# Optimization experiments

Measured on AMD Instinct MI355X. Metric: run time of the kernel, lower is better.

## Reference

```python
import jax, jax.numpy as jnp
import numpy as np

N_NODES = 50000
N_EDGES = 1000000
N_HID = 64
N_GRAPHS = 500
IN_DIM = 4


def setup_inputs() -> dict:
    key = jax.random.key(0)
    ks = jax.random.split(key, 10)
    x = jax.random.normal(ks[0], (N_NODES, IN_DIM), dtype=jnp.float32)
    edge_index = jax.random.randint(ks[1], (2, N_EDGES), 0, N_NODES, dtype=jnp.int64)
    batch = jnp.sort(jax.random.randint(ks[2], (N_NODES,), 0, N_GRAPHS, dtype=jnp.int64))
    # learned parameters (glorot-ish init)
    W1 = jax.random.normal(ks[3], (IN_DIM, N_HID), dtype=jnp.float32) / np.sqrt(IN_DIM)
    b1 = jnp.zeros((N_HID,), dtype=jnp.float32)
    W2 = jax.random.normal(ks[4], (N_HID, N_HID), dtype=jnp.float32) / np.sqrt(N_HID)
    b2 = jnp.zeros((N_HID,), dtype=jnp.float32)
    W3 = jax.random.normal(ks[5], (N_HID, 1), dtype=jnp.float32) / np.sqrt(N_HID)
    b3 = jnp.zeros((1,), dtype=jnp.float32)
    return {"x": x, "edge_index": edge_index, "batch": batch,
            "W1": W1, "b1": b1, "W2": W2, "b2": b2, "W3": W3, "b3": b3}


def gcn_conv(x, W, b, src, dst, num_nodes):
    """PyG GCNConv: x@W, add self-loops, sym deg^-1/2 norm, scatter-add aggregate, +bias."""
    h = x @ W  # [N, D]
    loop = jnp.arange(num_nodes, dtype=src.dtype)
    s = jnp.concatenate([src, loop])  # source nodes (messages gathered from)
    d = jnp.concatenate([dst, loop])  # target nodes (messages scattered to)
    deg = jax.ops.segment_sum(jnp.ones_like(d, dtype=h.dtype), d, num_segments=num_nodes)
    dis = jnp.where(deg > 0, jax.lax.rsqrt(jnp.maximum(deg, 1e-12)), 0.0)
    norm = dis[s] * dis[d]  # [E+N]
    msg = h[s] * norm[:, None]  # gather + scale: the memory-bound hot loop
    out = jax.ops.segment_sum(msg, d, num_segments=num_nodes)
    return out + b


def reference(x, edge_index, batch, W1, b1, W2, b2, W3, b3):
    src, dst = edge_index[0], edge_index[1]
    n = x.shape[0]
    h = gcn_conv(x, W1, b1, src, dst, n)
    h = jax.nn.elu(h)
    # F.dropout with training=False (eval mode) is identity
    h = gcn_conv(h, W2, b2, src, dst, n)
    h = jax.nn.elu(h)
    # scatter-mean pooling over graphs
    sums = jax.ops.segment_sum(h, batch, num_segments=N_GRAPHS)
    cnts = jax.ops.segment_sum(jnp.ones((n,), dtype=h.dtype), batch, num_segments=N_GRAPHS)
    pooled = sums / jnp.maximum(cnts, 1.0)[:, None]
    return pooled @ W3 + b3  # [N_GRAPHS, 1]
```

## Files before the change

### kernel.cpp

```cpp
#include <hip/hip_runtime.h>
#include <math.h>

#define N_NODES 50000
#define N_EDGES 1000000
#define N_HID 64
#define N_GRAPHS 500
#define IN_DIM 4
#define NPAD 50048

#define BK_SHIFT 7
#define BK_NODES 128
#define NBUCK 391
#define BCAP 3072
#define EPT 16
#define EPW (EPT * 256)
#define NWG_BIN ((N_EDGES + EPW - 1) / EPW)

__global__ void k_init(int* bcur, int* gstart, int* gend) {
    int i = threadIdx.x;
    if (i < 512) { bcur[i] = 0; gstart[i] = 0; gend[i] = 0; }
}

__global__ void k_bin(const int* __restrict__ ei, int* bcur, int* __restrict__ P) {
    __shared__ int hist[NBUCK];
    __shared__ int base[NBUCK];
    int t = threadIdx.x;
    int wg0 = blockIdx.x * EPW;
    for (int b = t; b < NBUCK; b += 256) hist[b] = 0;
    __syncthreads();

    const int4* s4 = (const int4*)ei;
    const int4* d4 = (const int4*)(ei + N_EDGES);
    int rs[EPT], rd[EPT];
#pragma unroll
    for (int i = 0; i < 4; ++i) {
        int e = wg0 + (i * 256 + t) * 4;
        if (e < N_EDGES) {
            int4 vs = s4[e >> 2];
            int4 vd = d4[e >> 2];
            rs[i * 4 + 0] = vs.x; rd[i * 4 + 0] = vd.x;
            rs[i * 4 + 1] = vs.y; rd[i * 4 + 1] = vd.y;
            rs[i * 4 + 2] = vs.z; rd[i * 4 + 2] = vd.z;
            rs[i * 4 + 3] = vs.w; rd[i * 4 + 3] = vd.w;
            atomicAdd(&hist[vd.x >> BK_SHIFT], 1);
            atomicAdd(&hist[vd.y >> BK_SHIFT], 1);
            atomicAdd(&hist[vd.z >> BK_SHIFT], 1);
            atomicAdd(&hist[vd.w >> BK_SHIFT], 1);
        } else {
            rd[i * 4 + 0] = rd[i * 4 + 1] = rd[i * 4 + 2] = rd[i * 4 + 3] = -1;
        }
    }
    __syncthreads();
    for (int b = t; b < NBUCK; b += 256) {
        int h = hist[b];
        base[b] = h ? atomicAdd(&bcur[b], h) : 0;
    }
    __syncthreads();
    for (int b = t; b < NBUCK; b += 256) hist[b] = 0;
    __syncthreads();
#pragma unroll
    for (int i = 0; i < EPT; ++i) {
        if (rd[i] >= 0) {
            int bk = rd[i] >> BK_SHIFT;
            int loc = base[bk] + atomicAdd(&hist[bk], 1);
            if (loc > BCAP - 1) loc = BCAP - 1;
            P[(size_t)bk * BCAP + loc] = (rs[i] << BK_SHIFT) | (rd[i] & (BK_NODES - 1));
        }
    }
}

__global__ void k_build(const int* __restrict__ bcur, const int* __restrict__ P,
                        const float* __restrict__ x,
                        int* __restrict__ srcidx, int* __restrict__ offs,
                        int* __restrict__ endp, float* __restrict__ dis,
                        float* __restrict__ xs) {
    __shared__ int sp[BCAP];
    __shared__ int scnt[BK_NODES];
    __shared__ int sscan[BK_NODES];
    __shared__ int scur[BK_NODES];
    int b = blockIdx.x;
    int t = threadIdx.x;
    int n = bcur[b];
    if (n > BCAP) n = BCAP;
    if (t < BK_NODES) scnt[t] = 0;
    __syncthreads();
    for (int i = t; i < n; i += 256) {
        int v = P[(size_t)b * BCAP + i];
        sp[i] = v;
        atomicAdd(&scnt[v & (BK_NODES - 1)], 1);
    }
    __syncthreads();
    if (t < BK_NODES) sscan[t] = scnt[t];
    __syncthreads();
    for (int d = 1; d < BK_NODES; d <<= 1) {
        int v = 0;
        if (t < BK_NODES && t >= d) v = sscan[t - d];
        __syncthreads();
        if (t < BK_NODES) sscan[t] += v;
        __syncthreads();
    }
    if (t < BK_NODES) {
        int excl = sscan[t] - scnt[t];
        scur[t] = excl;
        int node = b * BK_NODES + t;
        if (node < N_NODES) {
            int o = b * BCAP + excl;
            offs[node] = o;
            endp[node] = o + scnt[t];
            float dd = 1.0f / sqrtf((float)(scnt[t] + 1));
            dis[node] = dd;
            float4 xv = ((const float4*)x)[node];
            xv.x *= dd; xv.y *= dd; xv.z *= dd; xv.w *= dd;
            ((float4*)xs)[node] = xv;
        }
    }
    __syncthreads();
    for (int i = t; i < n; i += 256) {
        int v = sp[i];
        int ln = v & (BK_NODES - 1);
        int pos = b * BCAP + atomicAdd(&scur[ln], 1);
        srcidx[pos] = v >> BK_SHIFT;
    }
}

__global__ void k_layer1(const float* __restrict__ xs, const int* __restrict__ offs,
                         const int* __restrict__ endp, const int* __restrict__ srcidx,
                         const float* __restrict__ dis, const int* __restrict__ batch,
                         const float* __restrict__ W1, const float* __restrict__ b1,
                         int* __restrict__ gstart, int* __restrict__ gend,
                         float* __restrict__ h1s) {
    __shared__ float4 sagg[256];
    __shared__ float sdis[256];
    __shared__ float sW1[IN_DIM * N_HID];
    __shared__ float sb1[N_HID];
    int t = threadIdx.x;
    int nb = blockIdx.x * 256;
    int i = nb + t;
    sW1[t] = W1[t];
    if (t < N_HID) sb1[t] = b1[t];
    if (i < N_NODES) {
        int g = batch[i];
        if (i == 0 || batch[i - 1] != g) gstart[g] = i;
        if (i == N_NODES - 1 || batch[i + 1] != g) gend[g] = i + 1;
        const float4* xs4 = (const float4*)xs;
        float4 a0 = xs4[i];
        float4 a1 = make_float4(0.f, 0.f, 0.f, 0.f);
        float4 a2 = a1, a3 = a1;
        int q = offs[i], e = endp[i];
        for (; q + 4 <= e; q += 4) {
            int i0 = srcidx[q], i1 = srcidx[q + 1], i2 = srcidx[q + 2], i3 = srcidx[q + 3];
            float4 v0 = xs4[i0], v1 = xs4[i1], v2 = xs4[i2], v3 = xs4[i3];
            a0.x += v0.x; a0.y += v0.y; a0.z += v0.z; a0.w += v0.w;
            a1.x += v1.x; a1.y += v1.y; a1.z += v1.z; a1.w += v1.w;
            a2.x += v2.x; a2.y += v2.y; a2.z += v2.z; a2.w += v2.w;
            a3.x += v3.x; a3.y += v3.y; a3.z += v3.z; a3.w += v3.w;
        }
        for (; q < e; ++q) {
            float4 v = xs4[srcidx[q]];
            a0.x += v.x; a0.y += v.y; a0.z += v.z; a0.w += v.w;
        }
        float dd = dis[i];
        float4 r;
        r.x = (a0.x + a1.x + a2.x + a3.x) * dd;
        r.y = (a0.y + a1.y + a2.y + a3.y) * dd;
        r.z = (a0.z + a1.z + a2.z + a3.z) * dd;
        r.w = (a0.w + a1.w + a2.w + a3.w) * dd;
        sagg[t] = r;
        sdis[t] = dd;
    } else {
        sagg[t] = make_float4(0.f, 0.f, 0.f, 0.f);
        sdis[t] = 0.f;
    }
    __syncthreads();
    int w = t >> 6, j = t & 63;
    float w0 = sW1[0 * N_HID + j], w1 = sW1[1 * N_HID + j];
    float w2 = sW1[2 * N_HID + j], w3 = sW1[3 * N_HID + j];
    float bj = sb1[j];
    for (int n = 0; n < 64; ++n) {
        int local = w * 64 + n;
        int node = nb + local;
        if (node >= N_NODES) break;
        float4 a = sagg[local];
        float acc = a.x * w0 + a.y * w1 + a.z * w2 + a.w * w3 + bj;
        acc = acc > 0.f ? acc : expm1f(acc);
        h1s[(size_t)node * N_HID + j] = acc * sdis[local];
    }
}

__global__ void k_agg(const float* __restrict__ hs, const int* __restrict__ offs,
                      const int* __restrict__ endp, const int* __restrict__ srcidx,
                      const float* __restrict__ dis, float* __restrict__ out) {
    int wid = (blockIdx.x * blockDim.x + threadIdx.x) >> 6;
    int lane = threadIdx.x & 63;
    int g = lane >> 4, l = lane & 15;
    if (wid >= N_NODES) return;
    const float4* hs4 = (const float4*)hs;
    int start = offs[wid], end = endp[wid];
    float4 a0 = make_float4(0.f, 0.f, 0.f, 0.f);
    float4 a1 = a0, a2 = a0, a3 = a0;
    if (g == 0) a0 = hs4[(size_t)wid * 16 + l];
    for (int base = start; base < end; base += 64) {
        int nc = end - base; if (nc > 64) nc = 64;
        int myidx = (base + lane < end) ? srcidx[base + lane] : 0;
        int q = 0;
        for (; q + 16 <= nc; q += 16) {
            int s0 = __shfl(myidx, q + g);
            int s1 = __shfl(myidx, q + 4 + g);
            int s2 = __shfl(myidx, q + 8 + g);
            int s3 = __shfl(myidx, q + 12 + g);
            float4 v0 = hs4[(size_t)s0 * 16 + l];
            float4 v1 = hs4[(size_t)s1 * 16 + l];
            float4 v2 = hs4[(size_t)s2 * 16 + l];
            float4 v3 = hs4[(size_t)s3 * 16 + l];
            a0.x += v0.x; a0.y += v0.y; a0.z += v0.z; a0.w += v0.w;
            a1.x += v1.x; a1.y += v1.y; a1.z += v1.z; a1.w += v1.w;
            a2.x += v2.x; a2.y += v2.y; a2.z += v2.z; a2.w += v2.w;
            a3.x += v3.x; a3.y += v3.y; a3.z += v3.z; a3.w += v3.w;
        }
        for (; q + 4 <= nc; q += 4) {
            int s = __shfl(myidx, q + g);
            float4 v = hs4[(size_t)s * 16 + l];
            a0.x += v.x; a0.y += v.y; a0.z += v.z; a0.w += v.w;
        }
        {
            int s = __shfl(myidx, q + g);
            if (q + g < nc) {
                float4 v = hs4[(size_t)s * 16 + l];
                a1.x += v.x; a1.y += v.y; a1.z += v.z; a1.w += v.w;
            }
        }
    }
    a0.x += a1.x + a2.x + a3.x; a0.y += a1.y + a2.y + a3.y;
    a0.z += a1.z + a2.z + a3.z; a0.w += a1.w + a2.w + a3.w;
    a0.x += __shfl_xor(a0.x, 16); a0.y += __shfl_xor(a0.y, 16);
    a0.z += __shfl_xor(a0.z, 16); a0.w += __shfl_xor(a0.w, 16);
    a0.x += __shfl_xor(a0.x, 32); a0.y += __shfl_xor(a0.y, 32);
    a0.z += __shfl_xor(a0.z, 32); a0.w += __shfl_xor(a0.w, 32);
    float dw = dis[wid];
    float4 r;
    r.x = a0.x * dw; r.y = a0.y * dw; r.z = a0.z * dw; r.w = a0.w * dw;
    if (g == 0) ((float4*)out)[(size_t)wid * 16 + l] = r;
}

#define GH_NODES 64
__global__ void k_gemm_hid(const float* __restrict__ act, const float* __restrict__ W2,
                           const float* __restrict__ b2, float* __restrict__ out) {
    __shared__ float sW[N_HID][N_HID];
    __shared__ float sAT[N_HID][68];
    int t = threadIdx.x;
    int nb = blockIdx.x * GH_NODES;
    {
        const float4* w4 = (const float4*)W2;
        float4* s4 = (float4*)&sW[0][0];
#pragma unroll
        for (int i = 0; i < 4; ++i) s4[t + 256 * i] = w4[t + 256 * i];
    }
    {
        int sn = t >> 2, k0 = (t & 3) * 16;
        int node = nb + sn;
        bool ok = node < N_NODES;
        const float4* a4 = (const float4*)&act[(size_t)(ok ? node : 0) * N_HID];
#pragma unroll
        for (int i = 0; i < 4; ++i) {
            float4 v = ok ? a4[k0 / 4 + i] : make_float4(0.f, 0.f, 0.f, 0.f);
            sAT[k0 + 4 * i + 0][sn] = v.x;
            sAT[k0 + 4 * i + 1][sn] = v.y;
            sAT[k0 + 4 * i + 2][sn] = v.z;
            sAT[k0 + 4 * i + 3][sn] = v.w;
        }
    }
    __syncthreads();
    int tj = t & 15, tn = t >> 4;
    float4 acc0 = make_float4(0.f, 0.f, 0.f, 0.f);
    float4 acc1 = acc0, acc2 = acc0, acc3 = acc0;
#pragma unroll 8
    for (int k = 0; k < N_HID; ++k) {
        float4 a = *(const float4*)&sAT[k][4 * tn];
        float4 w = *(const float4*)&sW[k][4 * tj];
        acc0.x += a.x * w.x; acc0.y += a.x * w.y; acc0.z += a.x * w.z; acc0.w += a.x * w.w;
        acc1.x += a.y * w.x; acc1.y += a.y * w.y; acc1.z += a.y * w.z; acc1.w += a.y * w.w;
        acc2.x += a.z * w.x; acc2.y += a.z * w.y; acc2.z += a.z * w.z; acc2.w += a.z * w.w;
        acc3.x += a.w * w.x; acc3.y += a.w * w.y; acc3.z += a.w * w.z; acc3.w += a.w * w.w;
    }
    float4 bb = ((const float4*)b2)[tj];
    float4* out4 = (float4*)out;
#define GH_FIN(ACC, I)                                                        \
    {                                                                         \
        int node = nb + 4 * tn + (I);                                         \
        if (node < N_NODES) {                                                 \
            float4 r;                                                         \
            r.x = ACC.x + bb.x; r.y = ACC.y + bb.y;                           \
            r.z = ACC.z + bb.z; r.w = ACC.w + bb.w;                           \
            r.x = r.x > 0.f ? r.x : expm1f(r.x);                              \
            r.y = r.y > 0.f ? r.y : expm1f(r.y);                              \
            r.z = r.z > 0.f ? r.z : expm1f(r.z);                              \
            r.w = r.w > 0.f ? r.w : expm1f(r.w);                              \
            out4[(size_t)node * 16 + tj] = r;                                 \
        }                                                                     \
    }
    GH_FIN(acc0, 0) GH_FIN(acc1, 1) GH_FIN(acc2, 2) GH_FIN(acc3, 3)
#undef GH_FIN
}

__global__ void k_pool_final(const float* __restrict__ h, const int* __restrict__ gstart,
                             const int* __restrict__ gend, const float* __restrict__ W3,
                             const float* __restrict__ b3, float* __restrict__ out) {
    __shared__ float part[4][N_HID];
    int g = blockIdx.x;
    int t = threadIdx.x;
    int w = t >> 6, j = t & 63;
    int s = gstart[g];
    int cnt = gend[g] - s;
    float acc = 0.f;
    for (int k = w; k < cnt; k += 4) acc += h[(size_t)(s + k) * N_HID + j];
    part[w][j] = acc;
    __syncthreads();
    if (w == 0) {
        float v = part[0][j] + part[1][j] + part[2][j] + part[3][j];
        v /= (float)(cnt > 0 ? cnt : 1);
        float p = v * W3[j];
#pragma unroll
        for (int off = 32; off; off >>= 1) p += __shfl_down(p, off);
        if (j == 0) out[g] = p + b3[0];
    }
}

extern "C" void kernel_launch(void* const* d_in, const int* in_sizes, int n_in,
                              void* d_out, int out_size, void* d_ws, size_t ws_size,
                              hipStream_t stream) {
    const float* x   = (const float*)d_in[0];
    const int*   ei  = (const int*)d_in[1];
    const int*   bat = (const int*)d_in[2];
    const float* W1  = (const float*)d_in[3];
    const float* b1  = (const float*)d_in[4];
    const float* W2  = (const float*)d_in[5];
    const float* b2  = (const float*)d_in[6];
    const float* W3  = (const float*)d_in[7];
    const float* b3  = (const float*)d_in[8];
    float* out = (float*)d_out;

    char* w = (char*)d_ws;
    int*   bcur   = (int*)w;   w += 512 * 4;
    int*   offs   = (int*)w;   w += NPAD * 4;
    int*   endp   = (int*)w;   w += NPAD * 4;
    float* dis    = (float*)w; w += NPAD * 4;
    int*   gstart = (int*)w;   w += 512 * 4;
    int*   gend   = (int*)w;   w += 512 * 4;
    float* xs     = (float*)w; w += (size_t)NPAD * IN_DIM * 4;
    int*   srcidx = (int*)w;   w += (size_t)NBUCK * BCAP * 4;
    float* bufA   = (float*)w; w += (size_t)N_NODES * N_HID * 4;
    float* bufB   = (float*)w; w += (size_t)N_NODES * N_HID * 4;
    int*   P      = (int*)bufB;

    const int B = 256;
    const int gN = (N_NODES + B - 1) / B;
    const int gW = (N_NODES * 64 + B - 1) / B;

    k_init<<<1, 512, 0, stream>>>(bcur, gstart, gend);
    k_bin<<<NWG_BIN, B, 0, stream>>>(ei, bcur, P);
    k_build<<<NBUCK, B, 0, stream>>>(bcur, P, x, srcidx, offs, endp, dis, xs);

    k_layer1<<<gN, B, 0, stream>>>(xs, offs, endp, srcidx, dis, bat, W1, b1,
                                   gstart, gend, bufA);

    k_agg<<<gW, B, 0, stream>>>(bufA, offs, endp, srcidx, dis, bufB);
    k_gemm_hid<<<(N_NODES + GH_NODES - 1) / GH_NODES, B, 0, stream>>>(bufB, W2, b2, bufA);

    k_pool_final<<<N_GRAPHS, B, 0, stream>>>(bufA, gstart, gend, W3, b3, out);
}
```

Baseline: 115.3 us.

## Fuse layer-2 aggregation, hidden GEMM, ELU and graph pooling into one kernel

```diff
diff --git a/kernel.cpp b/kernel.cpp
--- a/kernel.cpp
+++ b/kernel.cpp
@@ -16,9 +16,10 @@
 #define EPW (EPT * 256)
 #define NWG_BIN ((N_EDGES + EPW - 1) / EPW)
 
-__global__ void k_init(int* bcur, int* gstart, int* gend) {
-    int i = threadIdx.x;
+__global__ void k_init(int* bcur, int* gstart, int* gend, float* sums) {
+    int i = blockIdx.x * blockDim.x + threadIdx.x;
     if (i < 512) { bcur[i] = 0; gstart[i] = 0; gend[i] = 0; }
+    if (i < N_GRAPHS * N_HID) sums[i] = 0.f;
 }
 
 __global__ void k_bin(const int* __restrict__ ei, int* bcur, int* __restrict__ P) {
@@ -31,7 +32,7 @@
 
     const int4* s4 = (const int4*)ei;
     const int4* d4 = (const int4*)(ei + N_EDGES);
-    int rs[EPT], rd[EPT];
+    int rs[EPT], rd[EPT], rl[EPT];
 #pragma unroll
     for (int i = 0; i < 4; ++i) {
         int e = wg0 + (i * 256 + t) * 4;
@@ -42,10 +43,10 @@
             rs[i * 4 + 1] = vs.y; rd[i * 4 + 1] = vd.y;
             rs[i * 4 + 2] = vs.z; rd[i * 4 + 2] = vd.z;
             rs[i * 4 + 3] = vs.w; rd[i * 4 + 3] = vd.w;
-            atomicAdd(&hist[vd.x >> BK_SHIFT], 1);
-            atomicAdd(&hist[vd.y >> BK_SHIFT], 1);
-            atomicAdd(&hist[vd.z >> BK_SHIFT], 1);
-            atomicAdd(&hist[vd.w >> BK_SHIFT], 1);
+            rl[i * 4 + 0] = atomicAdd(&hist[vd.x >> BK_SHIFT], 1);
+            rl[i * 4 + 1] = atomicAdd(&hist[vd.y >> BK_SHIFT], 1);
+            rl[i * 4 + 2] = atomicAdd(&hist[vd.z >> BK_SHIFT], 1);
+            rl[i * 4 + 3] = atomicAdd(&hist[vd.w >> BK_SHIFT], 1);
         } else {
             rd[i * 4 + 0] = rd[i * 4 + 1] = rd[i * 4 + 2] = rd[i * 4 + 3] = -1;
         }
@@ -55,14 +56,12 @@
         int h = hist[b];
         base[b] = h ? atomicAdd(&bcur[b], h) : 0;
     }
-    __syncthreads();
-    for (int b = t; b < NBUCK; b += 256) hist[b] = 0;
     __syncthreads();
 #pragma unroll
     for (int i = 0; i < EPT; ++i) {
         if (rd[i] >= 0) {
             int bk = rd[i] >> BK_SHIFT;
-            int loc = base[bk] + atomicAdd(&hist[bk], 1);
+            int loc = base[bk] + rl[i];
             if (loc > BCAP - 1) loc = BCAP - 1;
             P[(size_t)bk * BCAP + loc] = (rs[i] << BK_SHIFT) | (rd[i] & (BK_NODES - 1));
         }
@@ -187,89 +186,83 @@
     }
 }
 
-__global__ void k_agg(const float* __restrict__ hs, const int* __restrict__ offs,
-                      const int* __restrict__ endp, const int* __restrict__ srcidx,
-                      const float* __restrict__ dis, float* __restrict__ out) {
-    int wid = (blockIdx.x * blockDim.x + threadIdx.x) >> 6;
-    int lane = threadIdx.x & 63;
-    int g = lane >> 4, l = lane & 15;
-    if (wid >= N_NODES) return;
-    const float4* hs4 = (const float4*)hs;
-    int start = offs[wid], end = endp[wid];
-    float4 a0 = make_float4(0.f, 0.f, 0.f, 0.f);
-    float4 a1 = a0, a2 = a0, a3 = a0;
-    if (g == 0) a0 = hs4[(size_t)wid * 16 + l];
-    for (int base = start; base < end; base += 64) {
-        int nc = end - base; if (nc > 64) nc = 64;
-        int myidx = (base + lane < end) ? srcidx[base + lane] : 0;
-        int q = 0;
-        for (; q + 16 <= nc; q += 16) {
-            int s0 = __shfl(myidx, q + g);
-            int s1 = __shfl(myidx, q + 4 + g);
-            int s2 = __shfl(myidx, q + 8 + g);
-            int s3 = __shfl(myidx, q + 12 + g);
-            float4 v0 = hs4[(size_t)s0 * 16 + l];
-            float4 v1 = hs4[(size_t)s1 * 16 + l];
-            float4 v2 = hs4[(size_t)s2 * 16 + l];
-            float4 v3 = hs4[(size_t)s3 * 16 + l];
-            a0.x += v0.x; a0.y += v0.y; a0.z += v0.z; a0.w += v0.w;
-            a1.x += v1.x; a1.y += v1.y; a1.z += v1.z; a1.w += v1.w;
-            a2.x += v2.x; a2.y += v2.y; a2.z += v2.z; a2.w += v2.w;
-            a3.x += v3.x; a3.y += v3.y; a3.z += v3.z; a3.w += v3.w;
-        }
-        for (; q + 4 <= nc; q += 4) {
-            int s = __shfl(myidx, q + g);
-            float4 v = hs4[(size_t)s * 16 + l];
-            a0.x += v.x; a0.y += v.y; a0.z += v.z; a0.w += v.w;
-        }
-        {
-            int s = __shfl(myidx, q + g);
-            if (q + g < nc) {
-                float4 v = hs4[(size_t)s * 16 + l];
-                a1.x += v.x; a1.y += v.y; a1.z += v.z; a1.w += v.w;
-            }
-        }
-    }
-    a0.x += a1.x + a2.x + a3.x; a0.y += a1.y + a2.y + a3.y;
-    a0.z += a1.z + a2.z + a3.z; a0.w += a1.w + a2.w + a3.w;
-    a0.x += __shfl_xor(a0.x, 16); a0.y += __shfl_xor(a0.y, 16);
-    a0.z += __shfl_xor(a0.z, 16); a0.w += __shfl_xor(a0.w, 16);
-    a0.x += __shfl_xor(a0.x, 32); a0.y += __shfl_xor(a0.y, 32);
-    a0.z += __shfl_xor(a0.z, 32); a0.w += __shfl_xor(a0.w, 32);
-    float dw = dis[wid];
-    float4 r;
-    r.x = a0.x * dw; r.y = a0.y * dw; r.z = a0.z * dw; r.w = a0.w * dw;
-    if (g == 0) ((float4*)out)[(size_t)wid * 16 + l] = r;
-}
-
-#define GH_NODES 64
-__global__ void k_gemm_hid(const float* __restrict__ act, const float* __restrict__ W2,
-                           const float* __restrict__ b2, float* __restrict__ out) {
+#define L2_NODES 64
+__global__ void k_layer2(const float* __restrict__ h1s, const int* __restrict__ offs,
+                         const int* __restrict__ endp, const int* __restrict__ srcidx,
+                         const float* __restrict__ dis, const int* __restrict__ batch,
+                         const float* __restrict__ W2, const float* __restrict__ b2,
+                         float* __restrict__ sums) {
     __shared__ float sW[N_HID][N_HID];
     __shared__ float sAT[N_HID][68];
+    __shared__ int sbat[L2_NODES];
     int t = threadIdx.x;
-    int nb = blockIdx.x * GH_NODES;
+    int nb = blockIdx.x * L2_NODES;
     {
         const float4* w4 = (const float4*)W2;
         float4* s4 = (float4*)&sW[0][0];
 #pragma unroll
         for (int i = 0; i < 4; ++i) s4[t + 256 * i] = w4[t + 256 * i];
     }
-    {
-        int sn = t >> 2, k0 = (t & 3) * 16;
-        int node = nb + sn;
-        bool ok = node < N_NODES;
-        const float4* a4 = (const float4*)&act[(size_t)(ok ? node : 0) * N_HID];
-#pragma unroll
-        for (int i = 0; i < 4; ++i) {
-            float4 v = ok ? a4[k0 / 4 + i] : make_float4(0.f, 0.f, 0.f, 0.f);
-            sAT[k0 + 4 * i + 0][sn] = v.x;
-            sAT[k0 + 4 * i + 1][sn] = v.y;
-            sAT[k0 + 4 * i + 2][sn] = v.z;
-            sAT[k0 + 4 * i + 3][sn] = v.w;
-        }
-    }
-    __syncthreads();
+    if (t < L2_NODES) sbat[t] = (nb + t < N_NODES) ? batch[nb + t] : -1;
+
+    int wv = t >> 6, lane = t & 63;
+    int g = lane >> 4, l = lane & 15;
+    const float4* hs4 = (const float4*)h1s;
+    for (int nn = 0; nn < 16; ++nn) {
+        int local = wv * 16 + nn;
+        int node = nb + local;
+        if (node >= N_NODES) break;
+        int start = offs[node], end = endp[node];
+        float4 a0 = make_float4(0.f, 0.f, 0.f, 0.f);
+        float4 a1 = a0, a2 = a0, a3 = a0;
+        if (g == 0) a0 = hs4[(size_t)node * 16 + l];
+        for (int base = start; base < end; base += 64) {
+            int nc = end - base; if (nc > 64) nc = 64;
+            int myidx = (base + lane < end) ? srcidx[base + lane] : 0;
+            int q = 0;
+            for (; q + 16 <= nc; q += 16) {
+                int s0 = __shfl(myidx, q + g);
+                int s1 = __shfl(myidx, q + 4 + g);
+                int s2 = __shfl(myidx, q + 8 + g);
+                int s3 = __shfl(myidx, q + 12 + g);
+                float4 v0 = hs4[(size_t)s0 * 16 + l];
+                float4 v1 = hs4[(size_t)s1 * 16 + l];
+                float4 v2 = hs4[(size_t)s2 * 16 + l];
+                float4 v3 = hs4[(size_t)s3 * 16 + l];
+                a0.x += v0.x; a0.y += v0.y; a0.z += v0.z; a0.w += v0.w;
+                a1.x += v1.x; a1.y += v1.y; a1.z += v1.z; a1.w += v1.w;
+                a2.x += v2.x; a2.y += v2.y; a2.z += v2.z; a2.w += v2.w;
+                a3.x += v3.x; a3.y += v3.y; a3.z += v3.z; a3.w += v3.w;
+            }
+            for (; q + 4 <= nc; q += 4) {
+                int s = __shfl(myidx, q + g);
+                float4 v = hs4[(size_t)s * 16 + l];
+                a0.x += v.x; a0.y += v.y; a0.z += v.z; a0.w += v.w;
+            }
+            {
+                int s = __shfl(myidx, q + g);
+                if (q + g < nc) {
+                    float4 v = hs4[(size_t)s * 16 + l];
+                    a1.x += v.x; a1.y += v.y; a1.z += v.z; a1.w += v.w;
+                }
+            }
+        }
+        a0.x += a1.x + a2.x + a3.x; a0.y += a1.y + a2.y + a3.y;
+        a0.z += a1.z + a2.z + a3.z; a0.w += a1.w + a2.w + a3.w;
+        a0.x += __shfl_xor(a0.x, 16); a0.y += __shfl_xor(a0.y, 16);
+        a0.z += __shfl_xor(a0.z, 16); a0.w += __shfl_xor(a0.w, 16);
+        a0.x += __shfl_xor(a0.x, 32); a0.y += __shfl_xor(a0.y, 32);
+        a0.z += __shfl_xor(a0.z, 32); a0.w += __shfl_xor(a0.w, 32);
+        if (g == 0) {
+            float dw = dis[node];
+            sAT[4 * l + 0][local] = a0.x * dw;
+            sAT[4 * l + 1][local] = a0.y * dw;
+            sAT[4 * l + 2][local] = a0.z * dw;
+            sAT[4 * l + 3][local] = a0.w * dw;
+        }
+    }
+    __syncthreads();
+
     int tj = t & 15, tn = t >> 4;
     float4 acc0 = make_float4(0.f, 0.f, 0.f, 0.f);
     float4 acc1 = acc0, acc2 = acc0, acc3 = acc0;
@@ -283,46 +276,52 @@
         acc3.x += a.w * w.x; acc3.y += a.w * w.y; acc3.z += a.w * w.z; acc3.w += a.w * w.w;
     }
     float4 bb = ((const float4*)b2)[tj];
-    float4* out4 = (float4*)out;
-#define GH_FIN(ACC, I)                                                        \
+    __syncthreads();
+#define L2_WB(ACC, I)                                                         \
     {                                                                         \
-        int node = nb + 4 * tn + (I);                                         \
-        if (node < N_NODES) {                                                 \
-            float4 r;                                                         \
-            r.x = ACC.x + bb.x; r.y = ACC.y + bb.y;                           \
-            r.z = ACC.z + bb.z; r.w = ACC.w + bb.w;                           \
-            r.x = r.x > 0.f ? r.x : expm1f(r.x);                              \
-            r.y = r.y > 0.f ? r.y : expm1f(r.y);                              \
-            r.z = r.z > 0.f ? r.z : expm1f(r.z);                              \
-            r.w = r.w > 0.f ? r.w : expm1f(r.w);                              \
-            out4[(size_t)node * 16 + tj] = r;                                 \
-        }                                                                     \
-    }
-    GH_FIN(acc0, 0) GH_FIN(acc1, 1) GH_FIN(acc2, 2) GH_FIN(acc3, 3)
-#undef GH_FIN
-}
-
-__global__ void k_pool_final(const float* __restrict__ h, const int* __restrict__ gstart,
-                             const int* __restrict__ gend, const float* __restrict__ W3,
-                             const float* __restrict__ b3, float* __restrict__ out) {
-    __shared__ float part[4][N_HID];
-    int g = blockIdx.x;
-    int t = threadIdx.x;
-    int w = t >> 6, j = t & 63;
-    int s = gstart[g];
-    int cnt = gend[g] - s;
-    float acc = 0.f;
-    for (int k = w; k < cnt; k += 4) acc += h[(size_t)(s + k) * N_HID + j];
-    part[w][j] = acc;
-    __syncthreads();
-    if (w == 0) {
-        float v = part[0][j] + part[1][j] + part[2][j] + part[3][j];
-        v /= (float)(cnt > 0 ? cnt : 1);
-        float p = v * W3[j];
+        float4 r;                                                             \
+        r.x = ACC.x + bb.x; r.y = ACC.y + bb.y;                               \
+        r.z = ACC.z + bb.z; r.w = ACC.w + bb.w;                               \
+        r.x = r.x > 0.f ? r.x : expm1f(r.x);                                  \
+        r.y = r.y > 0.f ? r.y : expm1f(r.y);                                  \
+        r.z = r.z > 0.f ? r.z : expm1f(r.z);                                  \
+        r.w = r.w > 0.f ? r.w : expm1f(r.w);                                  \
+        sAT[4 * tj + 0][4 * tn + (I)] = r.x;                                  \
+        sAT[4 * tj + 1][4 * tn + (I)] = r.y;                                  \
+        sAT[4 * tj + 2][4 * tn + (I)] = r.z;                                  \
+        sAT[4 * tj + 3][4 * tn + (I)] = r.w;                                  \
+    }
+    L2_WB(acc0, 0) L2_WB(acc1, 1) L2_WB(acc2, 2) L2_WB(acc3, 3)
+#undef L2_WB
+    __syncthreads();
+
+    int j = t & 63, w = t >> 6;
+    int s = 0;
+    while (s < L2_NODES) {
+        int gg = sbat[s];
+        int e = s + 1;
+        while (e < L2_NODES && sbat[e] == gg) ++e;
+        if (gg >= 0 && s + w < e) {
+            float p = 0.f;
+            for (int n = s + w; n < e; n += 4) p += sAT[j][n];
+            atomicAdd(&sums[gg * N_HID + j], p);
+        }
+        s = e;
+    }
+}
+
+__global__ void k_final(const float* __restrict__ sums, const int* __restrict__ gstart,
+                        const int* __restrict__ gend, const float* __restrict__ W3,
+                        const float* __restrict__ b3, float* __restrict__ out) {
+    int gid = blockIdx.x * 4 + (threadIdx.x >> 6);
+    int j = threadIdx.x & 63;
+    if (gid >= N_GRAPHS) return;
+    int cnt = gend[gid] - gstart[gid];
+    float v = sums[gid * N_HID + j] / (float)(cnt > 0 ? cnt : 1);
+    float p = v * W3[j];
 #pragma unroll
-        for (int off = 32; off; off >>= 1) p += __shfl_down(p, off);
-        if (j == 0) out[g] = p + b3[0];
-    }
+    for (int off = 32; off; off >>= 1) p += __shfl_down(p, off);
+    if (j == 0) out[gid] = p + b3[0];
 }
 
 extern "C" void kernel_launch(void* const* d_in, const int* in_sizes, int n_in,
@@ -346,25 +345,24 @@
     float* dis    = (float*)w; w += NPAD * 4;
     int*   gstart = (int*)w;   w += 512 * 4;
     int*   gend   = (int*)w;   w += 512 * 4;
+    float* sums   = (float*)w; w += (size_t)N_GRAPHS * N_HID * 4;
     float* xs     = (float*)w; w += (size_t)NPAD * IN_DIM * 4;
     int*   srcidx = (int*)w;   w += (size_t)NBUCK * BCAP * 4;
+    int*   P      = (int*)w;   w += (size_t)NBUCK * BCAP * 4;
     float* bufA   = (float*)w; w += (size_t)N_NODES * N_HID * 4;
-    float* bufB   = (float*)w; w += (size_t)N_NODES * N_HID * 4;
-    int*   P      = (int*)bufB;
 
     const int B = 256;
     const int gN = (N_NODES + B - 1) / B;
-    const int gW = (N_NODES * 64 + B - 1) / B;
-
-    k_init<<<1, 512, 0, stream>>>(bcur, gstart, gend);
+
+    k_init<<<(N_GRAPHS * N_HID + B - 1) / B, B, 0, stream>>>(bcur, gstart, gend, sums);
     k_bin<<<NWG_BIN, B, 0, stream>>>(ei, bcur, P);
     k_build<<<NBUCK, B, 0, stream>>>(bcur, P, x, srcidx, offs, endp, dis, xs);
 
     k_layer1<<<gN, B, 0, stream>>>(xs, offs, endp, srcidx, dis, bat, W1, b1,
                                    gstart, gend, bufA);
 
-    k_agg<<<gW, B, 0, stream>>>(bufA, offs, endp, srcidx, dis, bufB);
-    k_gemm_hid<<<(N_NODES + GH_NODES - 1) / GH_NODES, B, 0, stream>>>(bufB, W2, b2, bufA);
-
-    k_pool_final<<<N_GRAPHS, B, 0, stream>>>(bufA, gstart, gend, W3, b3, out);
-}
+    k_layer2<<<(N_NODES + L2_NODES - 1) / L2_NODES, B, 0, stream>>>(
+        bufA, offs, endp, srcidx, dis, bat, W2, b2, sums);
+
+    k_final<<<(N_GRAPHS + 3) / 4, B, 0, stream>>>(sums, gstart, gend, W3, b3, out);
+}
```

Result: faster. 110.0 us (-4.6%).
